# Kernel tuning notes

Measured on AMD Instinct MI355X. Metric: run time of the kernel, lower is better.

Reference implementation:

```python
import jax, jax.numpy as jnp
import numpy as np

B, N, C = 64, 512, 1280


def setup_inputs() -> dict:
    key = jax.random.key(0)
    ks = jax.random.split(key, 10)
    scale = 0.02
    x = jax.random.normal(ks[0], (B, N, C), dtype=jnp.float32)
    Mask = jax.random.randint(ks[1], (B, N, N), 0, 2, dtype=jnp.int32)
    Wq = jax.random.normal(ks[2], (C, C), dtype=jnp.float32) * scale
    bq = jnp.zeros((C,), dtype=jnp.float32)
    Wk = jax.random.normal(ks[3], (C, C), dtype=jnp.float32) * scale
    bk = jnp.zeros((C,), dtype=jnp.float32)
    Wv = jax.random.normal(ks[4], (C, C), dtype=jnp.float32) * scale
    bv = jnp.zeros((C,), dtype=jnp.float32)
    Wr = jax.random.normal(ks[5], (C, C), dtype=jnp.float32) * scale
    br = jnp.zeros((C,), dtype=jnp.float32)
    return {"x": x, "Mask": Mask, "Wq": Wq, "bq": bq, "Wk": Wk, "bk": bk,
            "Wv": Wv, "bv": bv, "Wr": Wr, "br": br}


def reference(x, Mask, Wq, bq, Wk, bk, Wv, bv, Wr, br):
    # q, k, v: [B, N, C]
    q = x @ Wq + bq
    k = x @ Wk + bk
    v = x @ Wv + bv
    # scores[b, n, m] = q[b, n] . k[b, m]  -> [B, N, N]
    scores = jnp.einsum('bnc,bmc->bnm', q, k)
    # masked_fill BEFORE the scale divide, as in the original module
    scores = jnp.where(Mask == 0, jnp.float32(-1e20), scores)
    attn = jax.nn.softmax(scores / jnp.sqrt(jnp.float32(C)), axis=-1)
    # original: (V^T @ attn).permute -> out[b, n, c] = sum_m v[b, m, c] * attn[b, m, n]
    att_feat = jnp.einsum('bmc,bmn->bnc', v, attn)
    return att_feat @ Wr + br
```

## Files before the change

kernel.cpp:

```cpp
#include <hip/hip_runtime.h>
#include <hip/hip_bf16.h>

#define DI __device__ __forceinline__

typedef __attribute__((ext_vector_type(8))) short short8;
typedef __attribute__((ext_vector_type(4))) float f32x4;

DI unsigned short f2bf(float f) {
    union { float f; unsigned int u; } v; v.f = f;
    unsigned int r = v.u + 0x7FFFu + ((v.u >> 16) & 1u);
    return (unsigned short)(r >> 16);
}
DI float bf2f(unsigned short h) {
    union { unsigned int u; float f; } v; v.u = ((unsigned int)h) << 16;
    return v.f;
}

#define GLD16(g, l) __builtin_amdgcn_global_load_lds( \
    (const __attribute__((address_space(1))) void*)(g), \
    (__attribute__((address_space(3))) void*)(l), 16, 0, 0)

template<int EPI, int QKV>
__global__ __launch_bounds__(512, 2) void gemm256(
    const unsigned short* __restrict__ A, const unsigned short* __restrict__ Bt,
    void* __restrict__ Cout, const float* __restrict__ bias,
    const float* __restrict__ bias1, const float* __restrict__ bias2,
    const int* __restrict__ mask, int K, int lda, int ldb, int ldc,
    long sA, long sB, long sC, long sM, float scale)
{
    __shared__ unsigned short lds[65536];

    const unsigned gx = gridDim.x, gy = gridDim.y;
    unsigned lin = blockIdx.x + gx * (blockIdx.y + gy * blockIdx.z);
    const unsigned nwg = gx * gy * gridDim.z;
    lin = (lin & 7u) * (nwg >> 3) + (lin >> 3);
    int tn = lin % gx;
    const int tm = (lin / gx) % gy;
    const int z = lin / (gx * gy);

    int gsel = 0;
    if (QKV) {
        gsel = tn / 5; tn -= gsel * 5;
        Bt += (size_t)gsel * sB;
        Cout = (void*)((unsigned short*)Cout + (size_t)gsel * sC);
        if (gsel == 1) bias = bias1; else if (gsel == 2) bias = bias2;
    }

    const unsigned short* Ab = A + (long)z * sA + (size_t)(tm * 256) * lda;
    const unsigned short* Bb = Bt + (QKV ? 0 : (long)z * sB) + (size_t)(tn * 256) * ldb;

    const int tid = threadIdx.x, wave = tid >> 6, l = tid & 63;
    const int wr = wave >> 2, wc = wave & 3;

    const int srow = wave * 32 + (l >> 2);
    const int schunk = ((l & 3) ^ ((l >> 3) & 3)) * 8;
    const unsigned short* agS = Ab + (size_t)srow * lda + schunk;
    const unsigned short* bgS = Bb + (size_t)srow * ldb + schunk;
    unsigned short* ldsA0 = &lds[wave * 1024];
    unsigned short* ldsB0 = &lds[8192 + wave * 1024];

    const int rl = l & 15;
    const int cl8 = ((l >> 4) ^ ((l >> 1) & 3)) * 8;
    const int aoff = (wr * 128 + rl) * 32 + cl8;
    const int boff = 8192 + (wc * 64 + rl) * 32 + cl8;

#define REGOFF(buf, h) (((buf) * 2 + (h)) * 16384)
#define SA(t, h, buf) { const unsigned short* g_ = agS + (size_t)((t) * 64 + (h) * 32); \
    GLD16(g_, ldsA0 + REGOFF(buf, h)); \
    GLD16(g_ + (size_t)16 * lda, ldsA0 + REGOFF(buf, h) + 512); }
#define SB(t, h, buf) { const unsigned short* g_ = bgS + (size_t)((t) * 64 + (h) * 32); \
    GLD16(g_, ldsB0 + REGOFF(buf, h)); \
    GLD16(g_ + (size_t)16 * ldb, ldsB0 + REGOFF(buf, h) + 512); }

    f32x4 acc[8][4] = {};

#define PHASE(buf, h, STG, VMW) { \
    short8 af[8], bfv[4]; \
    _Pragma("unroll") for (int i = 0; i < 4; ++i) \
        af[i] = *(const short8*)&lds[REGOFF(buf, h) + aoff + i * 512]; \
    _Pragma("unroll") for (int n = 0; n < 4; ++n) \
        bfv[n] = *(const short8*)&lds[REGOFF(buf, h) + boff + n * 512]; \
    _Pragma("unroll") for (int i = 4; i < 8; ++i) \
        af[i] = *(const short8*)&lds[REGOFF(buf, h) + aoff + i * 512]; \
    STG; \
    __builtin_amdgcn_s_setprio(1); \
    _Pragma("unroll") for (int i = 0; i < 8; ++i) \
        _Pragma("unroll") for (int n = 0; n < 4; ++n) \
            acc[i][n] = __builtin_amdgcn_mfma_f32_16x16x32_bf16( \
                af[i], bfv[n], acc[i][n], 0, 0, 0); \
    __builtin_amdgcn_s_setprio(0); \
    asm volatile("s_waitcnt " VMW ::: "memory"); \
    __builtin_amdgcn_s_barrier(); \
  }

    SA(0, 0, 0); SB(0, 0, 0); SA(0, 1, 0); SB(0, 1, 0); SA(1, 0, 1); SB(1, 0, 1);
    asm volatile("s_waitcnt vmcnt(8)" ::: "memory");
    __builtin_amdgcn_s_barrier();

    const int NI = K >> 7;
    for (int j = 0; j < NI - 1; ++j) {
        const int t = 2 * j;
        PHASE(0, 0, SA(t + 1, 1, 1) SB(t + 1, 1, 1), "vmcnt(8)")
        PHASE(0, 1, SA(t + 2, 0, 0) SB(t + 2, 0, 0), "vmcnt(8)")
        PHASE(1, 0, SA(t + 2, 1, 0) SB(t + 2, 1, 0), "vmcnt(8)")
        PHASE(1, 1, SA(t + 3, 0, 1) SB(t + 3, 0, 1), "vmcnt(8)")
    }
    {
        const int t = 2 * (NI - 1);
        PHASE(0, 0, SA(t + 1, 1, 1) SB(t + 1, 1, 1), "vmcnt(8)")
        PHASE(0, 1, ((void)0),                       "vmcnt(4)")
        PHASE(1, 0, ((void)0),                       "vmcnt(0)")
        PHASE(1, 1, ((void)0),                       "vmcnt(0)")
    }
#undef PHASE
#undef SA
#undef SB
#undef REGOFF

    const long cb = QKV ? 0 : (long)z * sC;
    const int row0 = tm * 256 + wr * 128 + (l >> 4) * 4;
    const int col0 = tn * 256 + wc * 64 + rl;

    if (QKV && gsel == 2) {
        float b4[4];
        #pragma unroll
        for (int n = 0; n < 4; ++n) b4[n] = bias[col0 + n * 16];
        unsigned short* vout = (unsigned short*)Cout;
        const int bz = tm >> 1, mb = (tm & 1) * 256;
        #pragma unroll
        for (int hc = 0; hc < 2; ++hc) {
            if ((wc >> 1) == hc) {
                #pragma unroll
                for (int mi = 0; mi < 8; ++mi)
                    #pragma unroll
                    for (int n = 0; n < 4; ++n)
                        #pragma unroll
                        for (int r = 0; r < 4; ++r) {
                            const int lc = (wc & 1) * 64 + n * 16 + rl;
                            const int m  = wr * 128 + mi * 16 + ((l >> 4) << 2) + r;
                            lds[lc * 264 + m] = f2bf(acc[mi][n][r] + b4[n]);
                        }
            }
            __syncthreads();
            #pragma unroll
            for (int rr = 0; rr < 8; ++rr) {
                const int row = rr * 16 + (tid >> 5);
                const int ch = tid & 31;
                short8 vv = *(const short8*)&lds[row * 264 + ch * 8];
                __builtin_nontemporal_store(vv,
                    (short8*)&vout[(size_t)bz * 655360
                        + (size_t)(tn * 256 + hc * 128 + row) * 512 + mb + ch * 8]);
            }
            __syncthreads();
        }
    } else if (EPI == 0) {
        float b4[4];
        #pragma unroll
        for (int n = 0; n < 4; ++n) b4[n] = bias[col0 + n * 16];
        unsigned short* gout = (unsigned short*)Cout;
        #pragma unroll
        for (int half = 0; half < 2; ++half) {
            if (wr == half) {
                #pragma unroll
                for (int mi = 0; mi < 8; ++mi)
                    #pragma unroll
                    for (int n = 0; n < 4; ++n)
                        #pragma unroll
                        for (int r = 0; r < 4; ++r) {
                            const int lr = mi * 16 + ((l >> 4) << 2) + r;
                            const int lc = wc * 64 + n * 16 + rl;
                            lds[lr * 264 + lc] = f2bf(acc[mi][n][r] + b4[n]);
                        }
            }
            __syncthreads();
            const long rbase = (long)(tm * 256 + half * 128);
            #pragma unroll
            for (int rr = 0; rr < 8; ++rr) {
                const int row = rr * 16 + (tid >> 5);
                const int ch = tid & 31;
                short8 vv = *(const short8*)&lds[row * 264 + ch * 8];
                __builtin_nontemporal_store(vv,
                    (short8*)&gout[(rbase + row) * (size_t)ldc + tn * 256 + ch * 8]);
            }
            __syncthreads();
        }
    } else {
        #pragma unroll
        for (int mi = 0; mi < 8; ++mi) {
            #pragma unroll
            for (int n = 0; n < 4; ++n) {
                #pragma unroll
                for (int r = 0; r < 4; ++r) {
                    const int row = row0 + mi * 16 + r;
                    const int col = col0 + n * 16;
                    float v = acc[mi][n][r];
                    if (EPI == 3) v += bias[col];
                    if (EPI == 1) {
                        v *= scale;
                        if (mask[(long)z * sM + (long)row * ldc + col] == 0)
                            v = -1e20f * scale;
                    }
                    if (EPI == 3)
                        __builtin_nontemporal_store(v, &((float*)Cout)[cb + (long)row * ldc + col]);
                    else
                        ((unsigned short*)Cout)[cb + (long)row * ldc + col] = f2bf(v);
                }
            }
        }
    }
}

__global__ void transpose_w(const float* __restrict__ Wq, const float* __restrict__ Wk,
                            const float* __restrict__ Wv, const float* __restrict__ Wr,
                            unsigned short* __restrict__ Wt)
{
    const float* W = blockIdx.z == 0 ? Wq : blockIdx.z == 1 ? Wk : blockIdx.z == 2 ? Wv : Wr;
    unsigned short* dst = Wt + (size_t)blockIdx.z * 1280 * 1280;
    __shared__ float T[64][65];
    const int j0 = blockIdx.x * 64, k0 = blockIdx.y * 64;
    const int tid = threadIdx.x;
    for (int it = 0; it < 16; ++it) {
        int idx = it * 256 + tid;
        int r = idx >> 6, c = idx & 63;
        T[r][c] = W[(size_t)(k0 + r) * 1280 + j0 + c];
    }
    __syncthreads();
    for (int it = 0; it < 16; ++it) {
        int idx = it * 256 + tid;
        int r = idx >> 6, c = idx & 63;
        dst[(size_t)(j0 + r) * 1280 + k0 + c] = f2bf(T[c][r]);
    }
}

__global__ void cast_x(const float* __restrict__ x, unsigned short* __restrict__ xb, long n)
{
    long i = ((long)blockIdx.x * 256 + threadIdx.x) * 8;
    if (i + 8 > n) return;
    const float4* p = (const float4*)(x + i);
    float4 a = p[0], b = p[1];
    unsigned short o[8] = { f2bf(a.x), f2bf(a.y), f2bf(a.z), f2bf(a.w),
                            f2bf(b.x), f2bf(b.y), f2bf(b.z), f2bf(b.w) };
    *(short8*)(xb + i) = *(short8*)o;
}

#define SMS 514
__global__ void softmax_t(const unsigned short* __restrict__ S, unsigned short* __restrict__ Pt)
{
    __shared__ unsigned short T[64 * SMS];
    __shared__ float rmax[64], rinv[64];
    const int b = blockIdx.y, mb = blockIdx.x * 64;
    const int tid = threadIdx.x, lane = tid & 63, wave = tid >> 6;
    const unsigned short* src = S + ((size_t)b * 512 + mb) * 512;

    for (int rr = 0; rr < 16; ++rr) {
        int r = rr * 4 + wave;
        const unsigned int* s = (const unsigned int*)(src + (size_t)r * 512);
        unsigned int* t = (unsigned int*)&T[r * SMS];
        #pragma unroll
        for (int j = 0; j < 4; ++j) t[lane + j * 64] = s[lane + j * 64];
    }
    __syncthreads();

    {
        int r = tid >> 2, q = tid & 3;
        const unsigned short* row = &T[r * SMS + q * 128];
        float mx = -3.0e38f;
        for (int i = 0; i < 128; ++i) mx = fmaxf(mx, bf2f(row[i]));
        mx = fmaxf(mx, __shfl_xor(mx, 1));
        mx = fmaxf(mx, __shfl_xor(mx, 2));
        float s = 0.f;
        for (int i = 0; i < 128; ++i) s += expf(bf2f(row[i]) - mx);
        s += __shfl_xor(s, 1);
        s += __shfl_xor(s, 2);
        if (q == 0) { rmax[r] = mx; rinv[r] = 1.0f / s; }
    }
    __syncthreads();

    {
        int m = tid & 63, nq = tid >> 6;
        float mxm = rmax[m], rim = rinv[m];
        unsigned short* dst = Pt + (size_t)b * 512 * 512 + mb + m;
        for (int it = 0; it < 128; ++it) {
            int n = it * 4 + nq;
            float v = expf(bf2f(T[m * SMS + n]) - mxm) * rim;
            dst[(size_t)n * 512] = f2bf(v);
        }
    }
}

extern "C" void kernel_launch(void* const* d_in, const int* in_sizes, int n_in,
                              void* d_out, int out_size, void* d_ws, size_t ws_size,
                              hipStream_t stream)
{
    const float* x   = (const float*)d_in[0];
    const int*  Mask = (const int*)d_in[1];
    const float* Wq  = (const float*)d_in[2];
    const float* bq  = (const float*)d_in[3];
    const float* Wk  = (const float*)d_in[4];
    const float* bk  = (const float*)d_in[5];
    const float* Wv  = (const float*)d_in[6];
    const float* bv  = (const float*)d_in[7];
    const float* Wr  = (const float*)d_in[8];
    const float* br  = (const float*)d_in[9];

    constexpr int N = 512, C = 1280;
    constexpr long MN = 32768;

    char* ws = (char*)d_ws;
    unsigned short* xb = (unsigned short*)ws;
    unsigned short* Wt = (unsigned short*)(ws + 83886080);
    unsigned short* Q  = (unsigned short*)(ws + 83886080 + 13107200);
    unsigned short* Km = Q + 41943040;
    unsigned short* VtD = Km + 41943040;
    unsigned short* Sp = VtD + 41943040;
    unsigned short* Pt = Sp + 16777216;
    unsigned short* att = xb;

    const float scale = 0.02795084971874737f;

    transpose_w<<<dim3(20, 20, 4), 256, 0, stream>>>(Wq, Wk, Wv, Wr, Wt);
    cast_x<<<dim3(20480), 256, 0, stream>>>(x, xb, MN * C);

    gemm256<0, 1><<<dim3(15, 128, 1), 512, 0, stream>>>(xb, Wt, (void*)Q, bq, bk, bv,
        nullptr, C, C, C, C, 0, 1638400L, 41943040L, 0, 0.f);

    gemm256<1, 0><<<dim3(2, 2, 64), 512, 0, stream>>>(Q, Km, (void*)Sp, nullptr, nullptr, nullptr,
        Mask, C, C, C, N, (long)N * C, (long)N * C, (long)N * N, (long)N * N, scale);

    softmax_t<<<dim3(8, 64), 256, 0, stream>>>(Sp, Pt);

    gemm256<2, 0><<<dim3(5, 2, 64), 512, 0, stream>>>(Pt, VtD, (void*)att, nullptr, nullptr, nullptr,
        nullptr, N, N, N, C, (long)N * N, (long)C * N, (long)N * C, 0, 0.f);

    gemm256<3, 0><<<dim3(5, 128, 1), 512, 0, stream>>>(att, Wt + 3 * 1638400, d_out, br, nullptr, nullptr,
        nullptr, C, C, C, C, 0, 0, 0, 0, 0.f);
}
```

Before: 663.1 us.

## Fuse QK^T score GEMM with mask, softmax and transposed probability store

Replaces the separate masked score GEMM and the softmax/transpose kernel with one kernel. Each workgroup computes a full 128x512 row block of scores, applies the mask and scale, and does the row max and sum reductions in registers and LDS. It then writes the transposed bf16 probabilities directly, so the bf16 score matrix no longer makes a round trip through HBM. The cost is a grid of only 256 workgroups with a larger per-block tile, which lowers parallelism. It also computes softmax from fp32 scores rather than bf16-rounded ones.

```diff
diff --git a/kernel.cpp b/kernel.cpp
--- a/kernel.cpp
+++ b/kernel.cpp
@@ -25,8 +25,8 @@
     const unsigned short* __restrict__ A, const unsigned short* __restrict__ Bt,
     void* __restrict__ Cout, const float* __restrict__ bias,
     const float* __restrict__ bias1, const float* __restrict__ bias2,
-    const int* __restrict__ mask, int K, int lda, int ldb, int ldc,
-    long sA, long sB, long sC, long sM, float scale)
+    int K, int lda, int ldb, int ldc,
+    long sA, long sB, long sC)
 {
     __shared__ unsigned short lds[65536];
 
@@ -195,17 +195,174 @@
                     const int col = col0 + n * 16;
                     float v = acc[mi][n][r];
                     if (EPI == 3) v += bias[col];
-                    if (EPI == 1) {
-                        v *= scale;
-                        if (mask[(long)z * sM + (long)row * ldc + col] == 0)
-                            v = -1e20f * scale;
-                    }
                     if (EPI == 3)
                         __builtin_nontemporal_store(v, &((float*)Cout)[cb + (long)row * ldc + col]);
                     else
                         ((unsigned short*)Cout)[cb + (long)row * ldc + col] = f2bf(v);
                 }
             }
+        }
+    }
+}
+
+__global__ __launch_bounds__(512, 2) void qk_softmax(
+    const unsigned short* __restrict__ Q, const unsigned short* __restrict__ Km,
+    unsigned short* __restrict__ Pt, const int* __restrict__ mask, float scale)
+{
+    __shared__ unsigned short lds[65536];
+
+    const unsigned gx = gridDim.x;
+    unsigned lin = blockIdx.x + gx * blockIdx.z;
+    const unsigned nwg = gx * gridDim.z;
+    lin = (lin & 7u) * (nwg >> 3) + (lin >> 3);
+    const int tm = lin % gx;
+    const int z  = lin / gx;
+
+    const unsigned short* Ab = Q  + (size_t)z * 655360 + (size_t)(tm * 128) * 1280;
+    const unsigned short* Bb = Km + (size_t)z * 655360;
+
+    const int tid = threadIdx.x, wave = tid >> 6, l = tid & 63;
+    const int wr = wave >> 2, wc = wave & 3;
+    const int rl = l & 15, lh = l >> 4;
+
+    const int schunk = ((l & 3) ^ ((l >> 3) & 3)) * 8;
+    const unsigned short* agS = Ab + (size_t)(wave * 16 + (l >> 2)) * 1280 + schunk;
+    const unsigned short* bgS = Bb + (size_t)(wave * 16 + (l >> 2)) * 1280 + schunk;
+    unsigned short* ldsA = &lds[wave * 512];
+    unsigned short* ldsB = &lds[4096 + wave * 512];
+
+    const int cl8 = ((l >> 4) ^ ((l >> 1) & 3)) * 8;
+    const int aoff = (wr * 64 + rl) * 32 + cl8;
+    const int boff = 4096 + (wc * 128 + rl) * 32 + cl8;
+
+#define SLOT(s) ((s) * 20480)
+#define SAQ(t, s) { GLD16(agS + (size_t)(t) * 32, ldsA + SLOT(s)); }
+#define SBQ(t, s) { const unsigned short* g_ = bgS + (size_t)(t) * 32; \
+    GLD16(g_,                       ldsB + SLOT(s)); \
+    GLD16(g_ + (size_t)128 * 1280,  ldsB + SLOT(s) + 4096); \
+    GLD16(g_ + (size_t)256 * 1280,  ldsB + SLOT(s) + 8192); \
+    GLD16(g_ + (size_t)384 * 1280,  ldsB + SLOT(s) + 12288); }
+
+    f32x4 acc[4][8] = {};
+
+    SAQ(0, 0) SBQ(0, 0) SAQ(1, 1) SBQ(1, 1)
+    asm volatile("s_waitcnt vmcnt(5)" ::: "memory");
+    __builtin_amdgcn_s_barrier();
+
+    int g0 = 0;
+    for (int t = 0; t < 40; ++t) {
+        const int base = g0 * 20480;
+        int g2 = g0 + 2; if (g2 >= 3) g2 -= 3;
+        const bool stg = (t + 2 < 40);
+        short8 af[4], bfv[8];
+        #pragma unroll
+        for (int i = 0; i < 4; ++i) af[i] = *(const short8*)&lds[base + aoff + i * 512];
+        #pragma unroll
+        for (int n = 0; n < 8; ++n) bfv[n] = *(const short8*)&lds[base + boff + n * 512];
+        if (stg) { SAQ(t + 2, g2) SBQ(t + 2, g2) }
+        __builtin_amdgcn_s_setprio(1);
+        #pragma unroll
+        for (int i = 0; i < 4; ++i)
+            #pragma unroll
+            for (int n = 0; n < 8; ++n)
+                acc[i][n] = __builtin_amdgcn_mfma_f32_16x16x32_bf16(af[i], bfv[n], acc[i][n], 0, 0, 0);
+        __builtin_amdgcn_s_setprio(0);
+        if (stg) { asm volatile("s_waitcnt vmcnt(5)" ::: "memory"); }
+        else     { asm volatile("s_waitcnt vmcnt(0)" ::: "memory"); }
+        __builtin_amdgcn_s_barrier();
+        g0 = (g0 == 2) ? 0 : g0 + 1;
+    }
+#undef SAQ
+#undef SBQ
+#undef SLOT
+
+    const int col0 = wc * 128 + rl;
+    {
+        const int* mb = mask + (size_t)z * 262144;
+        #pragma unroll
+        for (int mi = 0; mi < 4; ++mi)
+            #pragma unroll
+            for (int r = 0; r < 4; ++r) {
+                const int m = tm * 128 + wr * 64 + mi * 16 + lh * 4 + r;
+                const int* mp = mb + (size_t)m * 512 + col0;
+                #pragma unroll
+                for (int nj = 0; nj < 8; ++nj) {
+                    float x = acc[mi][nj][r] * scale;
+                    if (mp[nj * 16] == 0) x = -2.795084971874737e18f;
+                    acc[mi][nj][r] = x;
+                }
+            }
+    }
+    float* red = (float*)lds;
+    float rmx[4][4], rinv[4][4];
+    #pragma unroll
+    for (int mi = 0; mi < 4; ++mi)
+        #pragma unroll
+        for (int r = 0; r < 4; ++r) {
+            float mx = acc[mi][0][r];
+            #pragma unroll
+            for (int nj = 1; nj < 8; ++nj) mx = fmaxf(mx, acc[mi][nj][r]);
+            mx = fmaxf(mx, __shfl_xor(mx, 1));
+            mx = fmaxf(mx, __shfl_xor(mx, 2));
+            mx = fmaxf(mx, __shfl_xor(mx, 4));
+            mx = fmaxf(mx, __shfl_xor(mx, 8));
+            if (rl == 0) red[wc * 128 + wr * 64 + mi * 16 + lh * 4 + r] = mx;
+        }
+    __syncthreads();
+    #pragma unroll
+    for (int mi = 0; mi < 4; ++mi)
+        #pragma unroll
+        for (int r = 0; r < 4; ++r) {
+            const int rowl = wr * 64 + mi * 16 + lh * 4 + r;
+            rmx[mi][r] = fmaxf(fmaxf(red[rowl], red[128 + rowl]),
+                               fmaxf(red[256 + rowl], red[384 + rowl]));
+        }
+    __syncthreads();
+    #pragma unroll
+    for (int mi = 0; mi < 4; ++mi)
+        #pragma unroll
+        for (int r = 0; r < 4; ++r) {
+            float s = 0.f;
+            #pragma unroll
+            for (int nj = 0; nj < 8; ++nj) {
+                float e = __expf(acc[mi][nj][r] - rmx[mi][r]);
+                acc[mi][nj][r] = e; s += e;
+            }
+            s += __shfl_xor(s, 1); s += __shfl_xor(s, 2);
+            s += __shfl_xor(s, 4); s += __shfl_xor(s, 8);
+            if (rl == 0) red[wc * 128 + wr * 64 + mi * 16 + lh * 4 + r] = s;
+        }
+    __syncthreads();
+    #pragma unroll
+    for (int mi = 0; mi < 4; ++mi)
+        #pragma unroll
+        for (int r = 0; r < 4; ++r) {
+            const int rowl = wr * 64 + mi * 16 + lh * 4 + r;
+            rinv[mi][r] = 1.0f / (red[rowl] + red[128 + rowl] + red[256 + rowl] + red[384 + rowl]);
+        }
+    unsigned short* Pb = Pt + (size_t)z * 262144 + (size_t)tm * 128;
+    #pragma unroll
+    for (int nh = 0; nh < 2; ++nh) {
+        __syncthreads();
+        if ((wc >> 1) == nh) {
+            #pragma unroll
+            for (int mi = 0; mi < 4; ++mi)
+                #pragma unroll
+                for (int nj = 0; nj < 8; ++nj)
+                    #pragma unroll
+                    for (int r = 0; r < 4; ++r) {
+                        const int cl = (wc & 1) * 128 + nj * 16 + rl;
+                        const int rowl = wr * 64 + mi * 16 + lh * 4 + r;
+                        lds[cl * 132 + rowl] = f2bf(acc[mi][nj][r] * rinv[mi][r]);
+                    }
+        }
+        __syncthreads();
+        #pragma unroll
+        for (int rr = 0; rr < 8; ++rr) {
+            const int nl = rr * 32 + (tid >> 4);
+            const int ch = tid & 15;
+            short8 vv = *(const short8*)&lds[nl * 132 + ch * 8];
+            *(short8*)&Pb[(size_t)(nh * 256 + nl) * 512 + ch * 8] = vv;
         }
     }
 }
@@ -241,51 +398,6 @@
     unsigned short o[8] = { f2bf(a.x), f2bf(a.y), f2bf(a.z), f2bf(a.w),
                             f2bf(b.x), f2bf(b.y), f2bf(b.z), f2bf(b.w) };
     *(short8*)(xb + i) = *(short8*)o;
-}
-
-#define SMS 514
-__global__ void softmax_t(const unsigned short* __restrict__ S, unsigned short* __restrict__ Pt)
-{
-    __shared__ unsigned short T[64 * SMS];
-    __shared__ float rmax[64], rinv[64];
-    const int b = blockIdx.y, mb = blockIdx.x * 64;
-    const int tid = threadIdx.x, lane = tid & 63, wave = tid >> 6;
-    const unsigned short* src = S + ((size_t)b * 512 + mb) * 512;
-
-    for (int rr = 0; rr < 16; ++rr) {
-        int r = rr * 4 + wave;
-        const unsigned int* s = (const unsigned int*)(src + (size_t)r * 512);
-        unsigned int* t = (unsigned int*)&T[r * SMS];
-        #pragma unroll
-        for (int j = 0; j < 4; ++j) t[lane + j * 64] = s[lane + j * 64];
-    }
-    __syncthreads();
-
-    {
-        int r = tid >> 2, q = tid & 3;
-        const unsigned short* row = &T[r * SMS + q * 128];
-        float mx = -3.0e38f;
-        for (int i = 0; i < 128; ++i) mx = fmaxf(mx, bf2f(row[i]));
-        mx = fmaxf(mx, __shfl_xor(mx, 1));
-        mx = fmaxf(mx, __shfl_xor(mx, 2));
-        float s = 0.f;
-        for (int i = 0; i < 128; ++i) s += expf(bf2f(row[i]) - mx);
-        s += __shfl_xor(s, 1);
-        s += __shfl_xor(s, 2);
-        if (q == 0) { rmax[r] = mx; rinv[r] = 1.0f / s; }
-    }
-    __syncthreads();
-
-    {
-        int m = tid & 63, nq = tid >> 6;
-        float mxm = rmax[m], rim = rinv[m];
-        unsigned short* dst = Pt + (size_t)b * 512 * 512 + mb + m;
-        for (int it = 0; it < 128; ++it) {
-            int n = it * 4 + nq;
-            float v = expf(bf2f(T[m * SMS + n]) - mxm) * rim;
-            dst[(size_t)n * 512] = f2bf(v);
-        }
-    }
 }
 
 extern "C" void kernel_launch(void* const* d_in, const int* in_sizes, int n_in,
@@ -312,8 +424,7 @@
     unsigned short* Q  = (unsigned short*)(ws + 83886080 + 13107200);
     unsigned short* Km = Q + 41943040;
     unsigned short* VtD = Km + 41943040;
-    unsigned short* Sp = VtD + 41943040;
-    unsigned short* Pt = Sp + 16777216;
+    unsigned short* Pt = VtD + 41943040;
     unsigned short* att = xb;
 
     const float scale = 0.02795084971874737f;
@@ -322,16 +433,13 @@
     cast_x<<<dim3(20480), 256, 0, stream>>>(x, xb, MN * C);
 
     gemm256<0, 1><<<dim3(15, 128, 1), 512, 0, stream>>>(xb, Wt, (void*)Q, bq, bk, bv,
-        nullptr, C, C, C, C, 0, 1638400L, 41943040L, 0, 0.f);
-
-    gemm256<1, 0><<<dim3(2, 2, 64), 512, 0, stream>>>(Q, Km, (void*)Sp, nullptr, nullptr, nullptr,
-        Mask, C, C, C, N, (long)N * C, (long)N * C, (long)N * N, (long)N * N, scale);
-
-    softmax_t<<<dim3(8, 64), 256, 0, stream>>>(Sp, Pt);
+        C, C, C, C, 0, 1638400L, 41943040L);
+
+    qk_softmax<<<dim3(4, 1, 64), 512, 0, stream>>>(Q, Km, Pt, Mask, scale);
 
     gemm256<2, 0><<<dim3(5, 2, 64), 512, 0, stream>>>(Pt, VtD, (void*)att, nullptr, nullptr, nullptr,
-        nullptr, N, N, N, C, (long)N * N, (long)C * N, (long)N * C, 0, 0.f);
+        N, N, N, C, (long)N * N, (long)C * N, (long)N * C);
 
     gemm256<3, 0><<<dim3(5, 128, 1), 512, 0, stream>>>(att, Wt + 3 * 1638400, d_out, br, nullptr, nullptr,
-        nullptr, C, C, C, C, 0, 0, 0, 0, 0.f);
-}
+        C, C, C, C, 0, 0, 0);
+}
```

Result: faster. 645.8 us (median of 2 runs) (-2.6%).
